# Kernel optimization log

Hardware: AMD Instinct MI355X
Metric: run time of the kernel (lower is better)

The kernel has to match this reference:

```python
import math
import jax, jax.numpy as jnp
import numpy as np


def setup_inputs() -> dict:
    key = jax.random.key(0)
    kq, kk, kv = jax.random.split(key, 3)
    bs, n_tok, n_heads, width = 2, 2048, 8, 64
    deg = 32  # neighbors per dst token -> coo_cnt_max
    q = jax.random.normal(kq, (bs, n_tok, n_heads, width), dtype=jnp.float32)
    k = jax.random.normal(kk, (bs, n_tok, n_heads, width), dtype=jnp.float32)
    v = jax.random.normal(kv, (bs, n_tok, n_heads, width), dtype=jnp.float32)
    rng = np.random.default_rng(0)
    dst = np.repeat(np.arange(n_tok), deg)            # [cl]
    src = rng.integers(0, n_tok, size=n_tok * deg)    # [cl]
    sm = np.tile(np.arange(deg), n_tok)               # [cl], unique per dst
    coo = jnp.asarray(np.stack([dst, src, sm], axis=1), dtype=jnp.int32)  # [cl,3]
    return {"q": q, "k": k, "v": v, "coo": coo, "coo_cnt_max": deg}


def reference(q, k, v, coo, coo_cnt_max):
    bs, n_tok, n_heads, width = q.shape
    dst, src, sm = coo[:, 0], coo[:, 1], coo[:, 2]
    # [b, h, t, w] layout
    qq = q.transpose(0, 2, 1, 3)
    kk = k.transpose(0, 2, 1, 3)
    vv = v.transpose(0, 2, 1, 3)
    scale = -1.0 / math.sqrt(width)
    # per-edge negative scaled L1 distance: [b, h, cl]
    ww = jnp.sum(jnp.abs(qq[:, :, dst, :] - kk[:, :, src, :]), axis=-1) * scale
    neg_big = jnp.asarray(-1e32, dtype=q.dtype)
    # scatter edge scores into dense padded attention slots: [b, h, t, cnt+1]
    attn = jnp.full((bs, n_heads, n_tok, coo_cnt_max + 1), neg_big, dtype=q.dtype)
    attn = attn.at[:, :, dst, sm].set(ww)
    attn_sm = jax.nn.softmax(attn, axis=-1)
    # scatter values into padded neighbor-value tensor: [b, h, t, cnt+1, w]
    vw = jnp.zeros((bs, n_heads, n_tok, coo_cnt_max + 1, width), dtype=q.dtype)
    vw = vw.at[:, :, dst, sm, :].set(vv[:, :, src, :])
    vo = jnp.einsum('bhds,bhdsw->bdhw', attn_sm, vw)
    # only dst tokens appearing in coo receive output; others stay zero
    vout = jnp.zeros_like(v).at[:, dst, :, :].set(vo[:, dst, :, :])
    return vout
```

## Files before the change

### kernel.cpp

```cpp
#include <hip/hip_runtime.h>
#include <hip/hip_bf16.h>

#define BS   2
#define NT   2048
#define NH   8
#define WD   64
#define DEG  32

#define PK_ROWS   (BS * 4 * NT)
#define PK_ROW_B  512
#define PK_UINTS  (PK_ROWS * (PK_ROW_B / 4))

typedef _Float16 half2_t __attribute__((ext_vector_type(2)));

#if defined(__has_builtin)
#if __has_builtin(__builtin_amdgcn_fdot2)
#define HAVE_FDOT2 1
#endif
#endif

__device__ __forceinline__ unsigned short f2h(float f) {
    _Float16 h = (_Float16)f;
    unsigned short u; __builtin_memcpy(&u, &h, 2); return u;
}
__device__ __forceinline__ half2_t u2h2(unsigned int w) {
    half2_t r; __builtin_memcpy(&r, &w, 4); return r;
}
__device__ __forceinline__ unsigned int h22u(half2_t h) {
    unsigned int u; __builtin_memcpy(&u, &h, 4); return u;
}
__device__ __forceinline__ half2_t habs2(half2_t x) {
    unsigned int u = h22u(x) & 0x7fff7fffu;
    return u2h2(u);
}

__global__ __launch_bounds__(256) void pack_kv_f16(
    const float* __restrict__ k,
    const float* __restrict__ v,
    unsigned int* __restrict__ packed)
{
    const int u    = blockIdx.x * 256 + threadIdx.x;
    const int row  = u >> 7;
    const int pos  = u & 127;
    const int part = pos >> 6;
    const int e    = pos & 63;
    const int s    = row & (NT - 1);
    const int hp   = (row >> 11) & 3;
    const int b    = row >> 13;
    const int elem = e * 2;
    const int h_in = elem >> 6;
    const int w0   = elem & 63;

    const float* src = (part == 0 ? k : v)
        + (((size_t)(b * NT + s) * NH + hp * 2 + h_in) << 6) + w0;
    float2 f = *(const float2*)src;
    packed[u] = (unsigned int)f2h(f.x) | ((unsigned int)f2h(f.y) << 16);
}

__global__ __launch_bounds__(64) void l1attn_main_f16(
    const float* __restrict__ q,
    const unsigned int* __restrict__ packed,
    const int* __restrict__ coo,
    float* __restrict__ out)
{
    const int bid   = blockIdx.x;
    const int combo = bid & 7;
    const int hp    = combo & 3;
    const int b     = combo >> 2;
    const int t     = bid >> 3;
    const int ln    = threadIdx.x;
    const int hw    = ln >> 5;
    const int l     = ln & 31;

    __shared__ int          s_src[DEG];
    __shared__ unsigned int s_q[64];
    __shared__ unsigned int s_k[DEG * 64];

    if (ln < DEG) {
        s_src[ln] = coo[(t * DEG + ln) * 3 + 1];
    }
    {
        const float2* qrow = (const float2*)
            (q + ((size_t)(b * NT + t) * NH + hp * 2) * WD);
        float2 qv = qrow[ln];
        s_q[ln] = (unsigned int)f2h(qv.x) | ((unsigned int)f2h(qv.y) << 16);
    }
    __syncthreads();

    const size_t combo_base = (size_t)((b * 4 + hp) * NT) * (PK_ROW_B / 4);

    {
        const int rsub = ln >> 4;
        const int c    = ln & 15;
        #pragma unroll
        for (int r = 0; r < 8; ++r) {
            const int j = 4 * r + rsub;
            const int s = s_src[j];
            const int chunk = (c + j) & 15;
            const char* gaddr = (const char*)(packed + combo_base)
                              + (size_t)s * PK_ROW_B + chunk * 16;
            char* laddr = (char*)s_k + 4 * r * 256;
            __builtin_amdgcn_global_load_lds(
                (const __attribute__((address_space(1))) void*)gaddr,
                (__attribute__((address_space(3))) void*)laddr,
                16, 0, 0);
        }
    }

    const int jg = l >> 4;
    const int wq = l & 15;
    uint2 vr[16];
    {
        const char* vbase = (const char*)(packed + combo_base)
                          + (16 + hw * 8) * 16 + wq * 8;
        #pragma unroll
        for (int i = 0; i < 16; ++i) {
            const int sv = s_src[2 * i + jg];
            vr[i] = *(const uint2*)(vbase + (size_t)sv * PK_ROW_B);
        }
    }

    asm volatile("s_waitcnt vmcnt(16)" ::: "memory");

    float acc = 0.f;
#ifdef HAVE_FDOT2
    const half2_t one2 = {(_Float16)1.0f, (_Float16)1.0f};
#endif
    #pragma unroll
    for (int i = 0; i < 8; ++i) {
        const int slot = ((hw * 8 + i) - l) & 15;
        uint4 c = *(const uint4*)((const char*)s_k + l * 256 + slot * 16);
        const unsigned int ws[4] = {c.x, c.y, c.z, c.w};
        #pragma unroll
        for (int m = 0; m < 4; ++m) {
            half2_t kh = u2h2(ws[m]);
            half2_t qh = u2h2(s_q[hw * 32 + i * 4 + m]);
            half2_t ad = habs2(qh - kh);
#ifdef HAVE_FDOT2
            acc = __builtin_amdgcn_fdot2(ad, one2, acc, false);
#else
            acc += (float)ad.x + (float)ad.y;
#endif
        }
    }
    float logit = -0.125f * acc;

    float m = logit;
    #pragma unroll
    for (int d = 16; d >= 1; d >>= 1) m = fmaxf(m, __shfl_xor(m, d));
    float e = __expf(logit - m);
    float ssum = e;
    #pragma unroll
    for (int d = 16; d >= 1; d >>= 1) ssum += __shfl_xor(ssum, d);
    const float p = e / ssum;

    int p2i;
    {
        _Float16 ph = (_Float16)p;
        half2_t p2 = {ph, ph};
        p2i = h22u(p2);
    }
    half2_t a0 = {(_Float16)0.0f, (_Float16)0.0f};
    half2_t a1 = a0;
    #pragma unroll
    for (int i = 0; i < 16; ++i) {
        const int pj2i = __shfl(p2i, 2 * i + jg, 32);
        half2_t pj2 = u2h2(pj2i);
        a0 = __builtin_elementwise_fma(pj2, u2h2(vr[i].x), a0);
        a1 = __builtin_elementwise_fma(pj2, u2h2(vr[i].y), a1);
    }
    {
        unsigned int u0 = h22u(a0), u1 = h22u(a1);
        unsigned int o0 = __shfl_xor((int)u0, 16);
        unsigned int o1 = __shfl_xor((int)u1, 16);
        a0 = a0 + u2h2(o0);
        a1 = a1 + u2h2(o1);
    }

    if (jg == 0) {
        const int h = hp * 2 + hw;
        float4 res = make_float4((float)a0.x, (float)a0.y,
                                 (float)a1.x, (float)a1.y);
        *(float4*)(out + ((size_t)(b * NT + t) * NH + h) * WD + 4 * wq) = res;
    }
}

__global__ __launch_bounds__(64) void l1attn_sparse_fp32(
    const float* __restrict__ q,
    const float* __restrict__ k,
    const float* __restrict__ v,
    const int* __restrict__ coo,
    float* __restrict__ out)
{
    const int bid   = blockIdx.x;
    const int combo = bid & 7;
    const int hp    = combo & 3;
    const int b     = combo >> 2;
    const int t     = bid >> 3;
    const int ln    = threadIdx.x;
    const int hw    = ln >> 5;
    const int l     = ln & 31;

    __shared__ int   s_src[DEG];
    __shared__ float s_q[2 * WD];
    __shared__ float s_k[DEG * 2 * WD];

    if (ln < DEG) s_src[ln] = coo[(t * DEG + ln) * 3 + 1];
    {
        const float2* qrow = (const float2*)
            (q + ((size_t)(b * NT + t) * NH + hp * 2) * WD);
        float2 qv = qrow[ln];
        s_q[2 * ln] = qv.x; s_q[2 * ln + 1] = qv.y;
    }
    __syncthreads();
    {
        #pragma unroll
        for (int r = 0; r < 16; ++r) {
            const int j = 2 * r + hw;
            const int s = s_src[j];
            const int chunk = (l + j) & 31;
            const float* gaddr = k + ((size_t)(b * NT + s) * NH + hp * 2) * WD
                               + chunk * 4;
            float* laddr = s_k + 2 * r * (2 * WD);
            __builtin_amdgcn_global_load_lds(
                (const __attribute__((address_space(1))) void*)gaddr,
                (__attribute__((address_space(3))) void*)laddr, 16, 0, 0);
        }
    }
    const int h  = hp * 2 + hw;
    const int jg = l >> 4;
    const int wq = l & 15;
    float4 vr[16];
    #pragma unroll
    for (int i = 0; i < 16; ++i) {
        const int sv = s_src[2 * i + jg];
        vr[i] = *(const float4*)(v + ((size_t)(b * NT + sv) * NH + h) * WD + 4 * wq);
    }
    __syncthreads();
    const float* qh = s_q + hw * WD;
    float acc = 0.f;
    #pragma unroll
    for (int i = 0; i < 16; ++i) {
        const int slot = ((hw * 16 + i) - l) & 31;
        float4 kv = *(const float4*)(s_k + l * (2 * WD) + slot * 4);
        const int wb = i * 4;
        acc += fabsf(qh[wb] - kv.x) + fabsf(qh[wb + 1] - kv.y)
             + fabsf(qh[wb + 2] - kv.z) + fabsf(qh[wb + 3] - kv.w);
    }
    float logit = -0.125f * acc;
    float m = logit;
    #pragma unroll
    for (int d = 16; d >= 1; d >>= 1) m = fmaxf(m, __shfl_xor(m, d));
    float e = __expf(logit - m);
    float ssum = e;
    #pragma unroll
    for (int d = 16; d >= 1; d >>= 1) ssum += __shfl_xor(ssum, d);
    const float p = e / ssum;
    float4 o4 = make_float4(0.f, 0.f, 0.f, 0.f);
    #pragma unroll
    for (int i = 0; i < 16; ++i) {
        const float pj = __shfl(p, 2 * i + jg, 32);
        o4.x += pj * vr[i].x; o4.y += pj * vr[i].y;
        o4.z += pj * vr[i].z; o4.w += pj * vr[i].w;
    }
    o4.x += __shfl_xor(o4.x, 16); o4.y += __shfl_xor(o4.y, 16);
    o4.z += __shfl_xor(o4.z, 16); o4.w += __shfl_xor(o4.w, 16);
    if (jg == 0)
        *(float4*)(out + ((size_t)(b * NT + t) * NH + h) * WD + 4 * wq) = o4;
}

extern "C" void kernel_launch(void* const* d_in, const int* in_sizes, int n_in,
                              void* d_out, int out_size, void* d_ws, size_t ws_size,
                              hipStream_t stream) {
    const float* q   = (const float*)d_in[0];
    const float* k   = (const float*)d_in[1];
    const float* v   = (const float*)d_in[2];
    const int*   coo = (const int*)d_in[3];
    float*       o   = (float*)d_out;

    if (ws_size >= (size_t)PK_UINTS * 4) {
        unsigned int* packed = (unsigned int*)d_ws;
        hipLaunchKernelGGL(pack_kv_f16, dim3(PK_UINTS / 256), dim3(256), 0,
                           stream, k, v, packed);
        hipLaunchKernelGGL(l1attn_main_f16, dim3(BS * NT * 4), dim3(64), 0,
                           stream, q, packed, coo, o);
    } else {
        hipLaunchKernelGGL(l1attn_sparse_fp32, dim3(BS * NT * 4), dim3(64), 0,
                           stream, q, k, v, coo, o);
    }
}
```

Before: 96.79 us.

## Split head pair across two waves per block with wider V loads

The main kernel now launches 128 threads per block, with one 64-lane wave per head instead of one wave covering both heads with 32 lanes each. Each wave computes each edge score with two lanes plus a shuffle, and loads V as 16-byte chunks with 8 lanes per neighbor row. The aim is more lanes and loads in flight per block and fewer V-register loads per lane. The cost is extra cross-lane shuffle reductions and a larger block, which could change occupancy.

```diff
diff --git a/kernel.cpp b/kernel.cpp
--- a/kernel.cpp
+++ b/kernel.cpp
@@ -1,5 +1,4 @@
 #include <hip/hip_runtime.h>
-#include <hip/hip_bf16.h>
 
 #define BS   2
 #define NT   2048
@@ -57,7 +56,7 @@
     packed[u] = (unsigned int)f2h(f.x) | ((unsigned int)f2h(f.y) << 16);
 }
 
-__global__ __launch_bounds__(64) void l1attn_main_f16(
+__global__ __launch_bounds__(128, 8) void l1attn_2wave(
     const float* __restrict__ q,
     const unsigned int* __restrict__ packed,
     const int* __restrict__ coo,
@@ -68,120 +67,124 @@
     const int hp    = combo & 3;
     const int b     = combo >> 2;
     const int t     = bid >> 3;
-    const int ln    = threadIdx.x;
-    const int hw    = ln >> 5;
-    const int l     = ln & 31;
+    const int w     = threadIdx.x >> 6;
+    const int ln    = threadIdx.x & 63;
 
     __shared__ int          s_src[DEG];
-    __shared__ unsigned int s_q[64];
-    __shared__ unsigned int s_k[DEG * 64];
-
-    if (ln < DEG) {
+    __shared__ unsigned int s_q[2 * 32];
+    __shared__ unsigned int s_k[2 * DEG * 32];
+
+    if (w == 0 && ln < DEG) {
         s_src[ln] = coo[(t * DEG + ln) * 3 + 1];
     }
-    {
+    if (ln < 32) {
         const float2* qrow = (const float2*)
-            (q + ((size_t)(b * NT + t) * NH + hp * 2) * WD);
+            (q + ((size_t)(b * NT + t) * NH + hp * 2 + w) * WD);
         float2 qv = qrow[ln];
-        s_q[ln] = (unsigned int)f2h(qv.x) | ((unsigned int)f2h(qv.y) << 16);
+        s_q[w * 32 + ln] =
+            (unsigned int)f2h(qv.x) | ((unsigned int)f2h(qv.y) << 16);
     }
     __syncthreads();
 
-    const size_t combo_base = (size_t)((b * 4 + hp) * NT) * (PK_ROW_B / 4);
-
-    {
-        const int rsub = ln >> 4;
-        const int c    = ln & 15;
-        #pragma unroll
-        for (int r = 0; r < 8; ++r) {
-            const int j = 4 * r + rsub;
+    const char* pk = (const char*)packed
+                   + (size_t)((b * 4 + hp) * NT) * PK_ROW_B;
+
+    {
+        const int rsub = ln >> 3;
+        const int c    = ln & 7;
+        #pragma unroll
+        for (int r = 0; r < 4; ++r) {
+            const int j = 8 * r + rsub;
             const int s = s_src[j];
-            const int chunk = (c + j) & 15;
-            const char* gaddr = (const char*)(packed + combo_base)
-                              + (size_t)s * PK_ROW_B + chunk * 16;
-            char* laddr = (char*)s_k + 4 * r * 256;
+            const int chunk = (c + j) & 7;
+            const char* gaddr = pk + (size_t)s * PK_ROW_B
+                              + w * 128 + chunk * 16;
+            char* laddr = (char*)s_k + w * 4096 + r * 1024;
             __builtin_amdgcn_global_load_lds(
                 (const __attribute__((address_space(1))) void*)gaddr,
                 (__attribute__((address_space(3))) void*)laddr,
                 16, 0, 0);
         }
     }
-
-    const int jg = l >> 4;
-    const int wq = l & 15;
-    uint2 vr[16];
-    {
-        const char* vbase = (const char*)(packed + combo_base)
-                          + (16 + hw * 8) * 16 + wq * 8;
-        #pragma unroll
-        for (int i = 0; i < 16; ++i) {
-            const int sv = s_src[2 * i + jg];
-            vr[i] = *(const uint2*)(vbase + (size_t)sv * PK_ROW_B);
-        }
-    }
-
-    asm volatile("s_waitcnt vmcnt(16)" ::: "memory");
-
-    float acc = 0.f;
+    asm volatile("" ::: "memory");
+
+    const int jr = ln >> 3;
+    const int m8 = ln & 7;
+    uint4 vv[4];
+    {
+        const char* vbase = pk + 256 + w * 128 + m8 * 16;
+        #pragma unroll
+        for (int i = 0; i < 4; ++i) {
+            const int sv = s_src[8 * i + jr];
+            vv[i] = *(const uint4*)(vbase + (size_t)sv * PK_ROW_B);
+        }
+    }
+
+    asm volatile("s_waitcnt vmcnt(4)" ::: "memory");
+
+    const int j2  = ln >> 1;
+    const int h32 = ln & 1;
+    float a = 0.f;
 #ifdef HAVE_FDOT2
     const half2_t one2 = {(_Float16)1.0f, (_Float16)1.0f};
 #endif
     #pragma unroll
-    for (int i = 0; i < 8; ++i) {
-        const int slot = ((hw * 8 + i) - l) & 15;
-        uint4 c = *(const uint4*)((const char*)s_k + l * 256 + slot * 16);
-        const unsigned int ws[4] = {c.x, c.y, c.z, c.w};
+    for (int i = 0; i < 4; ++i) {
+        const int slot = ((4 * h32 + i) - j2) & 7;
+        uint4 c4 = *(const uint4*)
+            ((const char*)s_k + w * 4096 + j2 * 128 + slot * 16);
+        const unsigned int ws[4] = {c4.x, c4.y, c4.z, c4.w};
         #pragma unroll
         for (int m = 0; m < 4; ++m) {
             half2_t kh = u2h2(ws[m]);
-            half2_t qh = u2h2(s_q[hw * 32 + i * 4 + m]);
+            half2_t qh = u2h2(s_q[w * 32 + h32 * 16 + i * 4 + m]);
             half2_t ad = habs2(qh - kh);
 #ifdef HAVE_FDOT2
-            acc = __builtin_amdgcn_fdot2(ad, one2, acc, false);
+            a = __builtin_amdgcn_fdot2(ad, one2, a, false);
 #else
-            acc += (float)ad.x + (float)ad.y;
-#endif
-        }
-    }
-    float logit = -0.125f * acc;
-
-    float m = logit;
-    #pragma unroll
-    for (int d = 16; d >= 1; d >>= 1) m = fmaxf(m, __shfl_xor(m, d));
-    float e = __expf(logit - m);
-    float ssum = e;
-    #pragma unroll
-    for (int d = 16; d >= 1; d >>= 1) ssum += __shfl_xor(ssum, d);
-    const float p = e / ssum;
-
-    int p2i;
-    {
-        _Float16 ph = (_Float16)p;
-        half2_t p2 = {ph, ph};
-        p2i = h22u(p2);
-    }
-    half2_t a0 = {(_Float16)0.0f, (_Float16)0.0f};
-    half2_t a1 = a0;
-    #pragma unroll
-    for (int i = 0; i < 16; ++i) {
-        const int pj2i = __shfl(p2i, 2 * i + jg, 32);
-        half2_t pj2 = u2h2(pj2i);
-        a0 = __builtin_elementwise_fma(pj2, u2h2(vr[i].x), a0);
-        a1 = __builtin_elementwise_fma(pj2, u2h2(vr[i].y), a1);
-    }
-    {
-        unsigned int u0 = h22u(a0), u1 = h22u(a1);
-        unsigned int o0 = __shfl_xor((int)u0, 16);
-        unsigned int o1 = __shfl_xor((int)u1, 16);
-        a0 = a0 + u2h2(o0);
-        a1 = a1 + u2h2(o1);
-    }
-
-    if (jg == 0) {
-        const int h = hp * 2 + hw;
-        float4 res = make_float4((float)a0.x, (float)a0.y,
-                                 (float)a1.x, (float)a1.y);
-        *(float4*)(out + ((size_t)(b * NT + t) * NH + h) * WD + 4 * wq) = res;
+            a += (float)ad.x + (float)ad.y;
+#endif
+        }
+    }
+    a += __shfl_xor(a, 1);
+    float logit = -0.125f * a;
+
+    float mx = logit;
+    #pragma unroll
+    for (int d = 2; d <= 32; d <<= 1) mx = fmaxf(mx, __shfl_xor(mx, d));
+    float e = __expf(logit - mx);
+    float S = e;
+    #pragma unroll
+    for (int d = 2; d <= 32; d <<= 1) S += __shfl_xor(S, d);
+    const float p = e / S;
+
+    half2_t o0 = {(_Float16)0.0f, (_Float16)0.0f};
+    half2_t o1 = o0, o2 = o0, o3 = o0;
+    #pragma unroll
+    for (int i = 0; i < 4; ++i) {
+        const float pj = __shfl(p, 2 * (8 * i + jr));
+        const _Float16 ph = (_Float16)pj;
+        const half2_t p2 = {ph, ph};
+        o0 = __builtin_elementwise_fma(p2, u2h2(vv[i].x), o0);
+        o1 = __builtin_elementwise_fma(p2, u2h2(vv[i].y), o1);
+        o2 = __builtin_elementwise_fma(p2, u2h2(vv[i].z), o2);
+        o3 = __builtin_elementwise_fma(p2, u2h2(vv[i].w), o3);
+    }
+    #pragma unroll
+    for (int d = 8; d <= 32; d <<= 1) {
+        o0 = o0 + u2h2((unsigned int)__shfl_xor((int)h22u(o0), d));
+        o1 = o1 + u2h2((unsigned int)__shfl_xor((int)h22u(o1), d));
+        o2 = o2 + u2h2((unsigned int)__shfl_xor((int)h22u(o2), d));
+        o3 = o3 + u2h2((unsigned int)__shfl_xor((int)h22u(o3), d));
+    }
+
+    if (jr == 0) {
+        float* ob = out + ((size_t)(b * NT + t) * NH + hp * 2 + w) * WD
+                  + 8 * m8;
+        *(float4*)(ob)     = make_float4((float)o0.x, (float)o0.y,
+                                         (float)o1.x, (float)o1.y);
+        *(float4*)(ob + 4) = make_float4((float)o2.x, (float)o2.y,
+                                         (float)o3.x, (float)o3.y);
     }
 }
 
@@ -282,7 +285,7 @@
         unsigned int* packed = (unsigned int*)d_ws;
         hipLaunchKernelGGL(pack_kv_f16, dim3(PK_UINTS / 256), dim3(256), 0,
                            stream, k, v, packed);
-        hipLaunchKernelGGL(l1attn_main_f16, dim3(BS * NT * 4), dim3(64), 0,
+        hipLaunchKernelGGL(l1attn_2wave, dim3(BS * NT * 4), dim3(128), 0,
                            stream, q, packed, coo, o);
     } else {
         hipLaunchKernelGGL(l1attn_sparse_fp32, dim3(BS * NT * 4), dim3(64), 0,
```

Result: slower. 99.24 us (+2.5%).
